# Optimization experiments

Hardware: AMD Instinct MI355X
Metric: run time of the kernel (lower is better)

## Reference

```python
import jax, jax.numpy as jnp
import numpy as np

NUM_ENT = 100000
DIM = 768
BATCH = 4096
TAU = 0.05
ALPHA = 0.5
LARGE_NUM = 1e9


def setup_inputs() -> dict:
    key = jax.random.key(0)
    k1, k2 = jax.random.split(key)
    emb = jax.random.normal(k1, (NUM_ENT, DIM), dtype=jnp.float32)
    train_links = jax.random.randint(k2, (BATCH, 2), 0, NUM_ENT, dtype=jnp.int64)
    return {"emb": emb, "train_links": train_links}


def _soft_xent(logits, batch_size):
    # target is one-hot on column i for row i -> pick diagonal of log_softmax
    logprobs = jax.nn.log_softmax(logits, axis=1)
    diag = logprobs[jnp.arange(batch_size), jnp.arange(batch_size)]
    return -jnp.sum(diag) / batch_size


def reference(emb, train_links):
    # L2-normalize embeddings (norm=True default)
    emb_n = emb / jnp.linalg.norm(emb, axis=1, keepdims=True)
    h1 = emb_n[train_links[:, 0]]  # [B, D]
    h2 = emb_n[train_links[:, 1]]  # [B, D]
    B = h1.shape[0]
    mask = jnp.eye(B, dtype=h1.dtype) * LARGE_NUM

    logits_aa = jnp.matmul(h1, h1.T) / TAU - mask  # [B, B]
    logits_bb = jnp.matmul(h2, h2.T) / TAU - mask
    logits_ab = jnp.matmul(h1, h2.T) / TAU
    logits_ba = jnp.matmul(h2, h1.T) / TAU

    logits_a = jnp.concatenate([logits_ab, logits_aa], axis=1)  # [B, 2B]
    logits_b = jnp.concatenate([logits_ba, logits_bb], axis=1)

    loss_a = _soft_xent(logits_a, B)
    loss_b = _soft_xent(logits_b, B)
    return ALPHA * loss_a + (1.0 - ALPHA) * loss_b
```

## Files before the change

kernel.cpp:

```cpp
#include <hip/hip_runtime.h>
#include <hip/hip_bf16.h>
#include <math.h>

#define NUM_ENT 100000
#define DIM 768
#define BATCH 4096
#define INV_TAU 20.0f
#define QSCALE 16.0f
#define LOGIT_SCALE (INV_TAU / (QSCALE * QSCALE))

typedef __attribute__((ext_vector_type(4))) float f32x4;

__global__ __launch_bounds__(256) void gather_norm(
    const float* __restrict__ emb, const int* __restrict__ links,
    unsigned char* __restrict__ hn1, unsigned char* __restrict__ hn2)
{
    int rowId = blockIdx.x;
    int b     = rowId >> 1;
    int which = rowId & 1;
    int src   = links[2 * b + which];
    const float* srcRow = emb + (size_t)src * DIM;

    int t = threadIdx.x;
    float4 v = make_float4(0.f, 0.f, 0.f, 0.f);
    float ss = 0.f;
    if (t < DIM / 4) {
        v = ((const float4*)srcRow)[t];
        ss = v.x * v.x + v.y * v.y + v.z * v.z + v.w * v.w;
    }
    #pragma unroll
    for (int off = 32; off >= 1; off >>= 1) ss += __shfl_xor(ss, off);
    __shared__ float wsum[4];
    if ((t & 63) == 0) wsum[t >> 6] = ss;
    __syncthreads();
    float tot = wsum[0] + wsum[1] + wsum[2] + wsum[3];
    float scale = rsqrtf(tot) * QSCALE;

    if (t < DIM / 4) {
        unsigned char* dst = (which ? hn2 : hn1) + (size_t)b * DIM;
        int p = __builtin_amdgcn_cvt_pk_fp8_f32(v.x * scale, v.y * scale, 0, false);
        p     = __builtin_amdgcn_cvt_pk_fp8_f32(v.z * scale, v.w * scale, p, true);
        ((unsigned int*)dst)[t] = (unsigned int)p;
    }
}

__global__ __launch_bounds__(256) void gram_sym(
    const unsigned char* __restrict__ hn1, const unsigned char* __restrict__ hn2,
    float* __restrict__ S, float* __restrict__ diag)
{
    const int ct = blockIdx.x;
    const int rt = blockIdx.y;
    const int matId = blockIdx.z;
    if (matId > 0 && ct < rt) return;

    const unsigned char* A  = (matId == 2) ? hn2 : hn1;
    const unsigned char* Bm = (matId == 1) ? hn1 : hn2;
    const int  rowTarget = (matId == 2) ? 1 : 0;
    const int  colTarget = (matId == 1) ? 0 : 1;
    const bool maskDiag  = (matId > 0) && (rt == ct);
    const bool doColsum  = (matId == 0) || (rt != ct);
    const bool captureDiag = (matId == 0);

    __shared__ unsigned char sA[128 * 32];
    __shared__ unsigned char sB[128 * 32];

    const int t    = threadIdx.x;
    const int lane = t & 63;
    const int wave = t >> 6;
    const int wm   = wave >> 1, wn = wave & 1;
    const int quad = lane >> 4, l16 = lane & 15;
    const int row0 = rt * 128;
    const int col0 = ct * 128;

    f32x4 acc[4][4];
    #pragma unroll
    for (int im = 0; im < 4; ++im)
        #pragma unroll
        for (int jn = 0; jn < 4; ++jn)
            acc[im][jn] = (f32x4){0.f, 0.f, 0.f, 0.f};

    for (int kk = 0; kk < DIM; kk += 32) {
        {
            int r = t >> 1, h = t & 1;
            int koff = ((h + ((r >> 2) & 1)) & 1) * 16;
            const unsigned char* ga = A  + (size_t)(row0 + r) * DIM + kk + koff;
            const unsigned char* gb = Bm + (size_t)(col0 + r) * DIM + kk + koff;
            __builtin_amdgcn_global_load_lds(
                (const __attribute__((address_space(1))) void*)ga,
                (__attribute__((address_space(3))) void*)(sA + t * 16), 16, 0, 0);
            __builtin_amdgcn_global_load_lds(
                (const __attribute__((address_space(1))) void*)gb,
                (__attribute__((address_space(3))) void*)(sB + t * 16), 16, 0, 0);
        }
        __syncthreads();

        long long af[4], bfr[4];
        const int hk = quad >> 1, q8 = (quad & 1) * 8;
        #pragma unroll
        for (int im = 0; im < 4; ++im) {
            int row = wm * 64 + im * 16 + l16;
            int hl  = (hk + ((row >> 2) & 1)) & 1;
            af[im] = *(const long long*)&sA[row * 32 + hl * 16 + q8];
        }
        #pragma unroll
        for (int jn = 0; jn < 4; ++jn) {
            int row = wn * 64 + jn * 16 + l16;
            int hl  = (hk + ((row >> 2) & 1)) & 1;
            bfr[jn] = *(const long long*)&sB[row * 32 + hl * 16 + q8];
        }

        #pragma unroll
        for (int im = 0; im < 4; ++im)
            #pragma unroll
            for (int jn = 0; jn < 4; ++jn)
                acc[im][jn] = __builtin_amdgcn_mfma_f32_16x16x32_fp8_fp8(
                    af[im], bfr[jn], acc[im][jn], 0, 0, 0);
        __syncthreads();
    }

    float csum[4] = {0.f, 0.f, 0.f, 0.f};
    #pragma unroll
    for (int im = 0; im < 4; ++im) {
        #pragma unroll
        for (int r = 0; r < 4; ++r) {
            const int gi = row0 + wm * 64 + im * 16 + quad * 4 + r;
            float rsum = 0.f;
            #pragma unroll
            for (int jn = 0; jn < 4; ++jn) {
                const int gj = col0 + wn * 64 + jn * 16 + l16;
                float logit = acc[im][jn][r] * LOGIT_SCALE;
                bool isDiag = (gi == gj);
                if (captureDiag && isDiag) diag[gi] = logit;
                float e = __expf(logit);
                if (maskDiag && isDiag) e = 0.f;
                rsum += e;
                csum[jn] += e;
            }
            rsum += __shfl_xor(rsum, 1);
            rsum += __shfl_xor(rsum, 2);
            rsum += __shfl_xor(rsum, 4);
            rsum += __shfl_xor(rsum, 8);
            if (l16 == 0) atomicAdd(&S[rowTarget * BATCH + gi], rsum);
        }
    }
    if (doColsum) {
        #pragma unroll
        for (int jn = 0; jn < 4; ++jn) {
            float c = csum[jn];
            c += __shfl_xor(c, 16);
            c += __shfl_xor(c, 32);
            if (quad == 0) {
                const int gj = col0 + wn * 64 + jn * 16 + l16;
                atomicAdd(&S[colTarget * BATCH + gj], c);
            }
        }
    }
}

__global__ __launch_bounds__(256) void finalize(
    const float* __restrict__ S, const float* __restrict__ diag,
    float* __restrict__ out)
{
    int t = threadIdx.x;
    float local = 0.f;
    for (int i = t; i < BATCH; i += 256) {
        float lse_a = logf(S[i]);
        float lse_b = logf(S[BATCH + i]);
        local += 0.5f * (lse_a + lse_b) - diag[i];
    }
    #pragma unroll
    for (int off = 32; off >= 1; off >>= 1) local += __shfl_xor(local, off);
    __shared__ float wsum[4];
    if ((t & 63) == 0) wsum[t >> 6] = local;
    __syncthreads();
    if (t == 0) out[0] = (wsum[0] + wsum[1] + wsum[2] + wsum[3]) / (float)BATCH;
}

extern "C" void kernel_launch(void* const* d_in, const int* in_sizes, int n_in,
                              void* d_out, int out_size, void* d_ws, size_t ws_size,
                              hipStream_t stream)
{
    const float* emb  = (const float*)d_in[0];
    const int* links  = (const int*)d_in[1];

    char* ws = (char*)d_ws;
    unsigned char* hn1 = (unsigned char*)ws;
    unsigned char* hn2 = (unsigned char*)(ws + (size_t)BATCH * DIM);
    float* S    = (float*)(ws + (size_t)BATCH * DIM * 2);
    float* diag = (float*)(ws + (size_t)BATCH * DIM * 2 + 2 * BATCH * 4);

    hipMemsetAsync(S, 0, 2 * BATCH * sizeof(float), stream);

    gather_norm<<<dim3(2 * BATCH), 256, 0, stream>>>(emb, links, hn1, hn2);
    gram_sym<<<dim3(32, 32, 3), 256, 0, stream>>>(hn1, hn2, S, diag);
    finalize<<<1, 256, 0, stream>>>(S, diag, (float*)d_out);
}
```

Baseline: 430.1 us.

## Use 16x16x128 scaled FP8 MFMA with a deeper K tile

```diff
diff --git a/kernel.cpp b/kernel.cpp
--- a/kernel.cpp
+++ b/kernel.cpp
@@ -10,6 +10,8 @@
 #define LOGIT_SCALE (INV_TAU / (QSCALE * QSCALE))
 
 typedef __attribute__((ext_vector_type(4))) float f32x4;
+typedef __attribute__((ext_vector_type(8))) int   i32x8;
+#define UNIT_SCALE 0x7f7f7f7f
 
 __global__ __launch_bounds__(256) void gather_norm(
     const float* __restrict__ emb, const int* __restrict__ links,
@@ -61,8 +63,8 @@
     const bool doColsum  = (matId == 0) || (rt != ct);
     const bool captureDiag = (matId == 0);
 
-    __shared__ unsigned char sA[128 * 32];
-    __shared__ unsigned char sB[128 * 32];
+    __shared__ unsigned char sA[128 * 128];
+    __shared__ unsigned char sB[128 * 128];
 
     const int t    = threadIdx.x;
     const int lane = t & 63;
@@ -79,42 +81,47 @@
         for (int jn = 0; jn < 4; ++jn)
             acc[im][jn] = (f32x4){0.f, 0.f, 0.f, 0.f};
 
-    for (int kk = 0; kk < DIM; kk += 32) {
-        {
-            int r = t >> 1, h = t & 1;
-            int koff = ((h + ((r >> 2) & 1)) & 1) * 16;
-            const unsigned char* ga = A  + (size_t)(row0 + r) * DIM + kk + koff;
-            const unsigned char* gb = Bm + (size_t)(col0 + r) * DIM + kk + koff;
+    for (int kk = 0; kk < DIM; kk += 128) {
+        #pragma unroll
+        for (int rd = 0; rd < 4; ++rd) {
+            int idx = rd * 256 + t;
+            int r   = idx >> 3;
+            int p   = idx & 7;
+            int c   = (p - r) & 7;
+            const unsigned char* ga = A  + (size_t)(row0 + r) * DIM + kk + c * 16;
+            const unsigned char* gb = Bm + (size_t)(col0 + r) * DIM + kk + c * 16;
             __builtin_amdgcn_global_load_lds(
                 (const __attribute__((address_space(1))) void*)ga,
-                (__attribute__((address_space(3))) void*)(sA + t * 16), 16, 0, 0);
+                (__attribute__((address_space(3))) void*)(sA + idx * 16), 16, 0, 0);
             __builtin_amdgcn_global_load_lds(
                 (const __attribute__((address_space(1))) void*)gb,
-                (__attribute__((address_space(3))) void*)(sB + t * 16), 16, 0, 0);
+                (__attribute__((address_space(3))) void*)(sB + idx * 16), 16, 0, 0);
         }
         __syncthreads();
 
-        long long af[4], bfr[4];
-        const int hk = quad >> 1, q8 = (quad & 1) * 8;
+        const int cb = quad * 2;
+        i32x8 bf[4];
+        #pragma unroll
+        for (int jn = 0; jn < 4; ++jn) {
+            int rr = wn * 64 + jn * 16 + l16;
+            const int4 x0 = *(const int4*)&sB[rr * 128 + ((cb + rr) & 7) * 16];
+            const int4 x1 = *(const int4*)&sB[rr * 128 + ((cb + 1 + rr) & 7) * 16];
+            bf[jn] = (i32x8){x0.x, x0.y, x0.z, x0.w, x1.x, x1.y, x1.z, x1.w};
+        }
         #pragma unroll
         for (int im = 0; im < 4; ++im) {
-            int row = wm * 64 + im * 16 + l16;
-            int hl  = (hk + ((row >> 2) & 1)) & 1;
-            af[im] = *(const long long*)&sA[row * 32 + hl * 16 + q8];
-        }
-        #pragma unroll
-        for (int jn = 0; jn < 4; ++jn) {
-            int row = wn * 64 + jn * 16 + l16;
-            int hl  = (hk + ((row >> 2) & 1)) & 1;
-            bfr[jn] = *(const long long*)&sB[row * 32 + hl * 16 + q8];
-        }
-
-        #pragma unroll
-        for (int im = 0; im < 4; ++im)
+            int rr = wm * 64 + im * 16 + l16;
+            const int4 x0 = *(const int4*)&sA[rr * 128 + ((cb + rr) & 7) * 16];
+            const int4 x1 = *(const int4*)&sA[rr * 128 + ((cb + 1 + rr) & 7) * 16];
+            i32x8 af = (i32x8){x0.x, x0.y, x0.z, x0.w, x1.x, x1.y, x1.z, x1.w};
             #pragma unroll
             for (int jn = 0; jn < 4; ++jn)
-                acc[im][jn] = __builtin_amdgcn_mfma_f32_16x16x32_fp8_fp8(
-                    af[im], bfr[jn], acc[im][jn], 0, 0, 0);
+                acc[im][jn] = __builtin_amdgcn_mfma_scale_f32_16x16x128_f8f6f4(
+                    af, bf[jn], acc[im][jn],
+                    0, 0,
+                    0, UNIT_SCALE,
+                    0, UNIT_SCALE);
+        }
         __syncthreads();
     }
 
```

After: 464.2 us. 7.9% more time.

## Double-buffer LDS tiles and deepen K step in FP8 gram kernel

Applied to the files above, without the earlier changes.

```diff
diff --git a/kernel.cpp b/kernel.cpp
--- a/kernel.cpp
+++ b/kernel.cpp
@@ -61,8 +61,8 @@
     const bool doColsum  = (matId == 0) || (rt != ct);
     const bool captureDiag = (matId == 0);
 
-    __shared__ unsigned char sA[128 * 32];
-    __shared__ unsigned char sB[128 * 32];
+    __shared__ unsigned char sA[2][2][128][32];
+    __shared__ unsigned char sB[2][2][128][32];
 
     const int t    = threadIdx.x;
     const int lane = t & 63;
@@ -79,56 +79,67 @@
         for (int jn = 0; jn < 4; ++jn)
             acc[im][jn] = (f32x4){0.f, 0.f, 0.f, 0.f};
 
-    for (int kk = 0; kk < DIM; kk += 32) {
-        {
-            int r = t >> 1, h = t & 1;
-            int koff = ((h + ((r >> 2) & 1)) & 1) * 16;
-            const unsigned char* ga = A  + (size_t)(row0 + r) * DIM + kk + koff;
-            const unsigned char* gb = Bm + (size_t)(col0 + r) * DIM + kk + koff;
+    const int r    = t >> 1;
+    const int h    = t & 1;
+    const int koff = ((h + ((r >> 2) & 1)) & 1) * 16;
+    const unsigned char* gA = A  + (size_t)(row0 + r) * DIM + koff;
+    const unsigned char* gB = Bm + (size_t)(col0 + r) * DIM + koff;
+
+    auto stage = [&](int buf, int kk) {
+        #pragma unroll
+        for (int kb = 0; kb < 2; ++kb) {
             __builtin_amdgcn_global_load_lds(
-                (const __attribute__((address_space(1))) void*)ga,
-                (__attribute__((address_space(3))) void*)(sA + t * 16), 16, 0, 0);
+                (const __attribute__((address_space(1))) void*)(gA + kk + kb * 32),
+                (__attribute__((address_space(3))) void*)&sA[buf][kb][r][h * 16], 16, 0, 0);
             __builtin_amdgcn_global_load_lds(
-                (const __attribute__((address_space(1))) void*)gb,
-                (__attribute__((address_space(3))) void*)(sB + t * 16), 16, 0, 0);
+                (const __attribute__((address_space(1))) void*)(gB + kk + kb * 32),
+                (__attribute__((address_space(3))) void*)&sB[buf][kb][r][h * 16], 16, 0, 0);
+        }
+    };
+
+    const int NT = DIM / 64;
+    stage(0, 0);
+    __syncthreads();
+
+    const int hk = quad >> 1, q8 = (quad & 1) * 8;
+    for (int it = 0; it < NT; ++it) {
+        const int buf = it & 1;
+        if (it + 1 < NT) stage(buf ^ 1, (it + 1) * 64);
+
+        #pragma unroll
+        for (int kb = 0; kb < 2; ++kb) {
+            long long bfr[4];
+            #pragma unroll
+            for (int jn = 0; jn < 4; ++jn) {
+                int row = wn * 64 + jn * 16 + l16;
+                int hl  = (hk + ((row >> 2) & 1)) & 1;
+                bfr[jn] = *(const long long*)&sB[buf][kb][row][hl * 16 + q8];
+            }
+            #pragma unroll
+            for (int im = 0; im < 4; ++im) {
+                int row = wm * 64 + im * 16 + l16;
+                int hl  = (hk + ((row >> 2) & 1)) & 1;
+                long long af = *(const long long*)&sA[buf][kb][row][hl * 16 + q8];
+                #pragma unroll
+                for (int jn = 0; jn < 4; ++jn)
+                    acc[im][jn] = __builtin_amdgcn_mfma_f32_16x16x32_fp8_fp8(
+                        af, bfr[jn], acc[im][jn], 0, 0, 0);
+            }
         }
         __syncthreads();
-
-        long long af[4], bfr[4];
-        const int hk = quad >> 1, q8 = (quad & 1) * 8;
-        #pragma unroll
-        for (int im = 0; im < 4; ++im) {
-            int row = wm * 64 + im * 16 + l16;
-            int hl  = (hk + ((row >> 2) & 1)) & 1;
-            af[im] = *(const long long*)&sA[row * 32 + hl * 16 + q8];
-        }
-        #pragma unroll
-        for (int jn = 0; jn < 4; ++jn) {
-            int row = wn * 64 + jn * 16 + l16;
-            int hl  = (hk + ((row >> 2) & 1)) & 1;
-            bfr[jn] = *(const long long*)&sB[row * 32 + hl * 16 + q8];
-        }
-
-        #pragma unroll
-        for (int im = 0; im < 4; ++im)
-            #pragma unroll
-            for (int jn = 0; jn < 4; ++jn)
-                acc[im][jn] = __builtin_amdgcn_mfma_f32_16x16x32_fp8_fp8(
-                    af[im], bfr[jn], acc[im][jn], 0, 0, 0);
-        __syncthreads();
     }
 
     float csum[4] = {0.f, 0.f, 0.f, 0.f};
     #pragma unroll
     for (int im = 0; im < 4; ++im) {
         #pragma unroll
-        for (int r = 0; r < 4; ++r) {
-            const int gi = row0 + wm * 64 + im * 16 + quad * 4 + r;
+        for (int rr = 0; rr < 4; ++rr) {
+            const int gi = row0 + wm * 64 + im * 16 + quad * 4 + rr;
             float rsum = 0.f;
             #pragma unroll
             for (int jn = 0; jn < 4; ++jn) {
                 const int gj = col0 + wn * 64 + jn * 16 + l16;
-                float logit = acc[im][jn][r] * LOGIT_SCALE;
+                float logit = acc[im][jn][rr] * LOGIT_SCALE;
                 bool isDiag = (gi == gj);
                 if (captureDiag && isDiag) diag[gi] = logit;
                 float e = __expf(logit);
```

After: 435.2 us. About the same (+1.2%).
